# Performance work log

Measured on AMD Instinct MI355X. Metric: run time of the kernel, lower is better.

The kernel has to match this reference:

```python
import jax, jax.numpy as jnp
import numpy as np

N_NODES = 50000
N_EDGES = 800000
N_FEAT = 128
HIDDEN = 256
N_GRAPHS = 256
N_CLASSES = 10
BN_EPS = 1e-5


def setup_inputs() -> dict:
    key = jax.random.key(0)
    ks = jax.random.split(key, 12)
    s = 1.0 / np.sqrt(HIDDEN)
    inp = {
        "x": jax.random.normal(ks[0], (N_NODES, N_FEAT), dtype=jnp.float32),
        "edge_index": jax.random.randint(ks[1], (2, N_EDGES), 0, N_NODES, dtype=jnp.int64),
        "batch": jnp.sort(jax.random.randint(ks[2], (N_NODES,), 0, N_GRAPHS, dtype=jnp.int64)),
        "conv1_w0": jax.random.normal(ks[3], (N_FEAT, HIDDEN), dtype=jnp.float32) / np.sqrt(N_FEAT),
        "conv1_b0": jnp.zeros((HIDDEN,), jnp.float32),
        "conv1_w1": jax.random.normal(ks[4], (HIDDEN, HIDDEN), dtype=jnp.float32) * s,
        "conv1_b1": jnp.zeros((HIDDEN,), jnp.float32),
        "conv1_bn_gamma": jnp.ones((HIDDEN,), jnp.float32),
        "conv1_bn_beta": jnp.zeros((HIDDEN,), jnp.float32),
        "conv1_bn_mean": jnp.zeros((HIDDEN,), jnp.float32),
        "conv1_bn_var": jnp.ones((HIDDEN,), jnp.float32),
        "convs_w0": jax.random.normal(ks[5], (3, HIDDEN, HIDDEN), dtype=jnp.float32) * s,
        "convs_b0": jnp.zeros((3, HIDDEN), jnp.float32),
        "convs_w1": jax.random.normal(ks[6], (3, HIDDEN, HIDDEN), dtype=jnp.float32) * s,
        "convs_b1": jnp.zeros((3, HIDDEN), jnp.float32),
        "convs_bn_gamma": jnp.ones((3, HIDDEN), jnp.float32),
        "convs_bn_beta": jnp.zeros((3, HIDDEN), jnp.float32),
        "convs_bn_mean": jnp.zeros((3, HIDDEN), jnp.float32),
        "convs_bn_var": jnp.ones((3, HIDDEN), jnp.float32),
        "eps": jnp.zeros((4,), jnp.float32),
        "lin1_w": jax.random.normal(ks[7], (HIDDEN, HIDDEN), dtype=jnp.float32) * s,
        "lin1_b": jnp.zeros((HIDDEN,), jnp.float32),
        "lin2_w": jax.random.normal(ks[8], (HIDDEN, N_CLASSES), dtype=jnp.float32) * s,
        "lin2_b": jnp.zeros((N_CLASSES,), jnp.float32),
    }
    return inp


def _gin_conv(x, src, dst, eps, w0, b0, w1, b1, g, be, m, v):
    # message = x[src]; aggregate = scatter_add at dst; update = MLP((1+eps)*x + aggr)
    aggr = jax.ops.segment_sum(x[src], dst, num_segments=N_NODES)
    h = (1.0 + eps) * x + aggr
    h = jax.nn.relu(h @ w0 + b0)
    h = jax.nn.relu(h @ w1 + b1)
    return (h - m) * jax.lax.rsqrt(v + BN_EPS) * g + be  # eval-mode BatchNorm1d


def reference(x, edge_index, batch,
              conv1_w0, conv1_b0, conv1_w1, conv1_b1,
              conv1_bn_gamma, conv1_bn_beta, conv1_bn_mean, conv1_bn_var,
              convs_w0, convs_b0, convs_w1, convs_b1,
              convs_bn_gamma, convs_bn_beta, convs_bn_mean, convs_bn_var,
              eps, lin1_w, lin1_b, lin2_w, lin2_b):
    src, dst = edge_index[0], edge_index[1]
    h = _gin_conv(x, src, dst, eps[0], conv1_w0, conv1_b0, conv1_w1, conv1_b1,
                  conv1_bn_gamma, conv1_bn_beta, conv1_bn_mean, conv1_bn_var)
    for i in range(convs_w0.shape[0]):
        h = _gin_conv(h, src, dst, eps[i + 1], convs_w0[i], convs_b0[i],
                      convs_w1[i], convs_b1[i], convs_bn_gamma[i], convs_bn_beta[i],
                      convs_bn_mean[i], convs_bn_var[i])
    # global_mean_pool over graph ids
    sums = jax.ops.segment_sum(h, batch, num_segments=N_GRAPHS)
    cnts = jax.ops.segment_sum(jnp.ones((N_NODES,), h.dtype), batch, num_segments=N_GRAPHS)
    pooled = sums / jnp.maximum(cnts, 1.0)[:, None]
    h = jax.nn.relu(pooled @ lin1_w + lin1_b)  # dropout is identity at inference
    logits = h @ lin2_w + lin2_b
    return jax.nn.log_softmax(logits, axis=-1)
```

## Files before the change

### kernel.cpp

```cpp
#include <hip/hip_runtime.h>
#include <hip/hip_bf16.h>

#define N_NODES 50000
#define N_EDGES 800000
#define N_FEAT 128
#define HIDDEN 256
#define N_GRAPHS 256
#define N_CLASSES 10

#define NBUCK ((N_NODES + 255) / 256)
#define EPB 2048
#define NBLK_S ((N_EDGES + EPB - 1) / EPB)

typedef __hip_bfloat16 bf16_t;
typedef short bf16x8 __attribute__((ext_vector_type(8)));
typedef float f32x4 __attribute__((ext_vector_type(4)));

__device__ inline float bfb2f(short s) {
    unsigned u = ((unsigned)(unsigned short)s) << 16;
    float f; __builtin_memcpy(&f, &u, 4); return f;
}
__device__ inline short f2bfb(float f) {
    bf16_t b = __float2bfloat16(f);
    short s; __builtin_memcpy(&s, &b, 2); return s;
}


__global__ __launch_bounds__(256) void bucket_hist_kernel(const int* __restrict__ ei,
                                                          unsigned* __restrict__ histG) {
    __shared__ unsigned lh[NBUCK];
    int t = threadIdx.x, j = blockIdx.x;
    for (int i = t; i < NBUCK; i += 256) lh[i] = 0;
    __syncthreads();
    int base = j * EPB;
    #pragma unroll
    for (int it = 0; it < EPB / 256; it++) {
        int e = base + it * 256 + t;
        if (e < N_EDGES) atomicAdd(&lh[(unsigned)ei[N_EDGES + e] >> 8], 1u);
    }
    __syncthreads();
    for (int i = t; i < NBUCK; i += 256) histG[(size_t)j * NBUCK + i] = lh[i];
}

__global__ __launch_bounds__(256) void bucket_scan_kernel(unsigned* __restrict__ histG,
                                                          unsigned* __restrict__ bucketBase) {
    __shared__ unsigned tmp[256];
    int t = threadIdx.x;
    unsigned run = 0;
    if (t < NBUCK) {
        for (int j = 0; j < NBLK_S; j++) {
            unsigned v = histG[(size_t)j * NBUCK + t];
            histG[(size_t)j * NBUCK + t] = run;
            run += v;
        }
    }
    unsigned v = (t < NBUCK) ? run : 0;
    tmp[t] = v;
    __syncthreads();
    for (int off = 1; off < 256; off <<= 1) {
        unsigned a = (t >= off) ? tmp[t - off] : 0u;
        __syncthreads();
        tmp[t] += a;
        __syncthreads();
    }
    unsigned base = tmp[t] - v;
    if (t < NBUCK) {
        bucketBase[t] = base;
        for (int j = 0; j < NBLK_S; j++) histG[(size_t)j * NBUCK + t] += base;
    }
    if (t == NBUCK - 1) bucketBase[NBUCK] = base + v;
}

__global__ __launch_bounds__(256) void bucket_scatter_kernel(const int* __restrict__ ei,
                                                             const unsigned* __restrict__ histG,
                                                             unsigned long long* __restrict__ ebuf) {
    __shared__ unsigned lcur[NBUCK];
    int t = threadIdx.x, j = blockIdx.x;
    for (int i = t; i < NBUCK; i += 256) lcur[i] = histG[(size_t)j * NBUCK + i];
    __syncthreads();
    int base = j * EPB;
    #pragma unroll
    for (int it = 0; it < EPB / 256; it++) {
        int e = base + it * 256 + t;
        if (e < N_EDGES) {
            unsigned src = (unsigned)ei[e];
            unsigned dst = (unsigned)ei[N_EDGES + e];
            unsigned pos = atomicAdd(&lcur[dst >> 8], 1u);
            ebuf[pos] = (unsigned long long)src | ((unsigned long long)dst << 32);
        }
    }
}

__global__ __launch_bounds__(256) void fine_fill_kernel(const unsigned long long* __restrict__ ebuf,
                                                        const unsigned* __restrict__ bucketBase,
                                                        unsigned* __restrict__ rowptr,
                                                        int* __restrict__ adj) {
    __shared__ unsigned ldeg[256], lcur[256], tmp[256];
    int b = blockIdx.x, t = threadIdx.x;
    unsigned sbase = bucketBase[b];
    int scnt = (int)(bucketBase[b + 1] - sbase);
    ldeg[t] = 0;
    __syncthreads();
    for (int k = t; k < scnt; k += 256) {
        unsigned dst = (unsigned)(ebuf[sbase + k] >> 32);
        atomicAdd(&ldeg[dst & 255], 1u);
    }
    __syncthreads();
    unsigned v = ldeg[t];
    tmp[t] = v;
    __syncthreads();
    for (int off = 1; off < 256; off <<= 1) {
        unsigned a = (t >= off) ? tmp[t - off] : 0u;
        __syncthreads();
        tmp[t] += a;
        __syncthreads();
    }
    unsigned exc = tmp[t] - v;
    lcur[t] = exc;
    int gnode = b * 256 + t;
    if (gnode < N_NODES) rowptr[gnode] = sbase + exc;
    if (b == NBUCK - 1 && t == 0) rowptr[N_NODES] = N_EDGES;
    __syncthreads();
    for (int k = t; k < scnt; k += 256) {
        unsigned long long p = ebuf[sbase + k];
        unsigned dst = (unsigned)(p >> 32);
        unsigned pos = atomicAdd(&lcur[dst & 255], 1u);
        adj[sbase + pos] = (int)(p & 0xffffffffu);
    }
}


__global__ __launch_bounds__(256) void convert_x_kernel(const float* __restrict__ x,
                                                        bf16_t* __restrict__ xb) {
    int i = blockIdx.x * 256 + threadIdx.x;
    if (i < N_NODES * N_FEAT / 4) {
        float4 v = reinterpret_cast<const float4*>(x)[i];
        short4 o;
        o.x = f2bfb(v.x); o.y = f2bfb(v.y); o.z = f2bfb(v.z); o.w = f2bfb(v.w);
        reinterpret_cast<short4*>(xb)[i] = o;
    }
}


__global__ __launch_bounds__(256) void prep_weights_kernel(
    const float* __restrict__ c1_w0, const float* __restrict__ c1_w1,
    const float* __restrict__ cs_w0, const float* __restrict__ cs_w1,
    bf16_t* __restrict__ wt)
{
    __shared__ float T[32][33];
    int z = blockIdx.z;
    const float* src; int K; size_t off;
    if (z == 0)      { src = c1_w0; K = N_FEAT;  off = 0; }
    else if (z == 1) { src = c1_w1; K = HIDDEN;  off = 32768; }
    else {
        int i = (z - 2) >> 1;
        src = (((z - 2) & 1) ? cs_w1 : cs_w0) + (size_t)i * HIDDEN * HIDDEN;
        K = HIDDEN;
        off = 32768 + (size_t)(z - 1) * 65536;
    }
    int k0 = blockIdx.x * 32, n0 = blockIdx.y * 32;
    if (k0 >= K) return;
    int t = threadIdx.x;
    int r = t >> 3, c4 = (t & 7) * 4;
    float4 v = *reinterpret_cast<const float4*>(src + (size_t)(k0 + r) * HIDDEN + n0 + c4);
    T[r][c4 + 0] = v.x; T[r][c4 + 1] = v.y; T[r][c4 + 2] = v.z; T[r][c4 + 3] = v.w;
    __syncthreads();
    int n = t >> 3, kc = (t & 7) * 4;
    short4 o;
    o.x = f2bfb(T[kc + 0][n]); o.y = f2bfb(T[kc + 1][n]);
    o.z = f2bfb(T[kc + 2][n]); o.w = f2bfb(T[kc + 3][n]);
    *reinterpret_cast<short4*>((short*)wt + off + (size_t)(n0 + n) * K + k0 + kc) = o;
}


__global__ __launch_bounds__(256) void aggregate1_kernel(
    const bf16_t* __restrict__ xb, const int* __restrict__ adj,
    const unsigned* __restrict__ rowptr, const float* __restrict__ eps_arr,
    bf16_t* __restrict__ out)
{
    int w = threadIdx.x >> 6, lane = threadIdx.x & 63;
    int n = blockIdx.x * 4 + w;
    if (n >= N_NODES) return;
    int q = lane >> 4, l4 = lane & 15;
    unsigned beg = rowptr[n], end = rowptr[n + 1];
    const short* xs = (const short*)xb;
    float acc[8] = {};
    unsigned e = beg;
    for (; e + 8 <= end; e += 8) {
        int s0 = adj[e + q];
        int s1 = adj[e + 4 + q];
        bf16x8 v0 = *reinterpret_cast<const bf16x8*>(xs + (unsigned)s0 * N_FEAT + l4 * 8);
        bf16x8 v1 = *reinterpret_cast<const bf16x8*>(xs + (unsigned)s1 * N_FEAT + l4 * 8);
        #pragma unroll
        for (int j = 0; j < 8; j++) acc[j] += bfb2f(v0[j]) + bfb2f(v1[j]);
    }
    for (; e + 4 <= end; e += 4) {
        int s0 = adj[e + q];
        bf16x8 v0 = *reinterpret_cast<const bf16x8*>(xs + (unsigned)s0 * N_FEAT + l4 * 8);
        #pragma unroll
        for (int j = 0; j < 8; j++) acc[j] += bfb2f(v0[j]);
    }
    int rem = (int)(end - e);
    if (q < rem) {
        bf16x8 v0 = *reinterpret_cast<const bf16x8*>(xs + (unsigned)adj[e + q] * N_FEAT + l4 * 8);
        #pragma unroll
        for (int j = 0; j < 8; j++) acc[j] += bfb2f(v0[j]);
    }
    if (q == 0) {
        bf16x8 sv = *reinterpret_cast<const bf16x8*>(xs + (unsigned)n * N_FEAT + l4 * 8);
        float ep = 1.f + eps_arr[0];
        #pragma unroll
        for (int j = 0; j < 8; j++) acc[j] += ep * bfb2f(sv[j]);
    }
    #pragma unroll
    for (int j = 0; j < 8; j++) {
        acc[j] += __shfl_xor(acc[j], 16);
        acc[j] += __shfl_xor(acc[j], 32);
    }
    if (lane < 16) {
        bf16x8 o;
        #pragma unroll
        for (int j = 0; j < 8; j++) o[j] = f2bfb(acc[j]);
        *reinterpret_cast<bf16x8*>((short*)out + (unsigned)n * N_FEAT + l4 * 8) = o;
    }
}


__global__ __launch_bounds__(256) void aggregate2_kernel(
    const bf16_t* __restrict__ x, const int* __restrict__ adj,
    const unsigned* __restrict__ rowptr, const float* __restrict__ eps_arr, int eps_idx,
    bf16_t* __restrict__ out)
{
    int w = threadIdx.x >> 6, lane = threadIdx.x & 63;
    int n = blockIdx.x * 4 + w;
    if (n >= N_NODES) return;
    int half = lane >> 5, l5 = lane & 31;
    unsigned beg = rowptr[n], end = rowptr[n + 1];
    const short* xs = (const short*)x;
    float acc[8] = {};
    unsigned e = beg;
    for (; e + 8 <= end; e += 8) {
        int s0 = adj[e + half];
        int s1 = adj[e + 2 + half];
        int s2 = adj[e + 4 + half];
        int s3 = adj[e + 6 + half];
        bf16x8 v0 = *reinterpret_cast<const bf16x8*>(xs + (unsigned)s0 * HIDDEN + l5 * 8);
        bf16x8 v1 = *reinterpret_cast<const bf16x8*>(xs + (unsigned)s1 * HIDDEN + l5 * 8);
        bf16x8 v2 = *reinterpret_cast<const bf16x8*>(xs + (unsigned)s2 * HIDDEN + l5 * 8);
        bf16x8 v3 = *reinterpret_cast<const bf16x8*>(xs + (unsigned)s3 * HIDDEN + l5 * 8);
        #pragma unroll
        for (int j = 0; j < 8; j++)
            acc[j] += (bfb2f(v0[j]) + bfb2f(v1[j])) + (bfb2f(v2[j]) + bfb2f(v3[j]));
    }
    for (; e + 2 <= end; e += 2) {
        int s0 = adj[e + half];
        bf16x8 v0 = *reinterpret_cast<const bf16x8*>(xs + (unsigned)s0 * HIDDEN + l5 * 8);
        #pragma unroll
        for (int j = 0; j < 8; j++) acc[j] += bfb2f(v0[j]);
    }
    if (e < end && half == 0) {
        bf16x8 v0 = *reinterpret_cast<const bf16x8*>(xs + (unsigned)adj[e] * HIDDEN + l5 * 8);
        #pragma unroll
        for (int j = 0; j < 8; j++) acc[j] += bfb2f(v0[j]);
    }
    if (half == 0) {
        bf16x8 sv = *reinterpret_cast<const bf16x8*>(xs + (unsigned)n * HIDDEN + l5 * 8);
        float ep = 1.f + eps_arr[eps_idx];
        #pragma unroll
        for (int j = 0; j < 8; j++) acc[j] += ep * bfb2f(sv[j]);
    }
    #pragma unroll
    for (int j = 0; j < 8; j++) acc[j] += __shfl_xor(acc[j], 32);
    if (half == 0) {
        bf16x8 o;
        #pragma unroll
        for (int j = 0; j < 8; j++) o[j] = f2bfb(acc[j]);
        *reinterpret_cast<bf16x8*>((short*)out + (unsigned)n * HIDDEN + l5 * 8) = o;
    }
}


#define GBM 128
#define GBN 128
#define GBK 64

__global__ __launch_bounds__(512) void gemm_bf16_kernel(
    const bf16_t* __restrict__ A, const bf16_t* __restrict__ Wt,
    const float* __restrict__ bias, bf16_t* __restrict__ C,
    int M, int K,
    const float* __restrict__ bn_g, const float* __restrict__ bn_b,
    const float* __restrict__ bn_m, const float* __restrict__ bn_v, int do_bn)
{
    __shared__ short lds[18432];
    short (*As)[72] = reinterpret_cast<short(*)[72]>(lds);
    short (*Bs)[72] = reinterpret_cast<short(*)[72]>(lds + 9216);
    short (*Cs)[136] = reinterpret_cast<short(*)[136]>(lds);

    int tid = threadIdx.x;
    int lane = tid & 63;
    int wave = tid >> 6;
    int wr = wave >> 2, wc = wave & 3;
    int row0 = blockIdx.x * GBM, col0 = blockIdx.y * GBN;

    int lrow = tid >> 3, lch = tid & 7;

    const short* Ab = (const short*)A;
    const short* Wb = (const short*)Wt;

    f32x4 acc[4][2] = {};

    for (int k0 = 0; k0 < K; k0 += GBK) {
        #pragma unroll
        for (int rr = 0; rr < 2; rr++) {
            int r = lrow + rr * 64;
            int arow = row0 + r;
            bf16x8 av = {};
            if (arow < M)
                av = *reinterpret_cast<const bf16x8*>(Ab + (size_t)arow * K + k0 + lch * 8);
            *reinterpret_cast<bf16x8*>(&As[r][lch * 8]) = av;
            bf16x8 bv = *reinterpret_cast<const bf16x8*>(Wb + (size_t)(col0 + r) * K + k0 + lch * 8);
            *reinterpret_cast<bf16x8*>(&Bs[r][lch * 8]) = bv;
        }
        __syncthreads();

        int fr = lane & 15, fk = (lane >> 4) * 8;
        #pragma unroll
        for (int ks = 0; ks < 2; ks++) {
            bf16x8 a[4], b[2];
            #pragma unroll
            for (int m = 0; m < 4; m++)
                a[m] = *reinterpret_cast<const bf16x8*>(&As[wr * 64 + m * 16 + fr][ks * 32 + fk]);
            #pragma unroll
            for (int n = 0; n < 2; n++)
                b[n] = *reinterpret_cast<const bf16x8*>(&Bs[wc * 32 + n * 16 + fr][ks * 32 + fk]);
            #pragma unroll
            for (int m = 0; m < 4; m++)
                #pragma unroll
                for (int n = 0; n < 2; n++)
                    acc[m][n] = __builtin_amdgcn_mfma_f32_16x16x32_bf16(a[m], b[n], acc[m][n], 0, 0, 0);
        }
        __syncthreads();
    }

    #pragma unroll
    for (int m = 0; m < 4; m++) {
        #pragma unroll
        for (int n = 0; n < 2; n++) {
            int rl = wr * 64 + m * 16 + (lane >> 4) * 4;
            int cl = wc * 32 + n * 16 + (lane & 15);
            int c = col0 + cl;
            float bi = bias[c];
            #pragma unroll
            for (int r = 0; r < 4; r++) {
                float v = acc[m][n][r] + bi;
                v = fmaxf(v, 0.f);
                if (do_bn) v = (v - bn_m[c]) * rsqrtf(bn_v[c] + 1e-5f) * bn_g[c] + bn_b[c];
                Cs[rl + r][cl] = f2bfb(v);
            }
        }
    }
    __syncthreads();
    int lr = tid >> 2, c16 = tid & 3;
    int r = row0 + lr;
    if (r < M) {
        short* Cb = (short*)C;
        #pragma unroll
        for (int cc = 0; cc < 4; cc++) {
            int ch = c16 + cc * 4;
            bf16x8 cv = *reinterpret_cast<const bf16x8*>(&Cs[lr][ch * 8]);
            *reinterpret_cast<bf16x8*>(Cb + (size_t)r * HIDDEN + col0 + ch * 8) = cv;
        }
    }
}


__global__ __launch_bounds__(256) void pool_kernel(const bf16_t* __restrict__ h,
                                                   const int* __restrict__ batch,
                                                   float* __restrict__ pooled) {
    __shared__ int sbs[2];
    __shared__ float red[4][HIDDEN];
    int g = blockIdx.x;
    if (threadIdx.x == 0) {
        int lo = 0, hi = N_NODES;
        while (lo < hi) { int mid = (lo + hi) >> 1; if (batch[mid] < g) lo = mid + 1; else hi = mid; }
        sbs[0] = lo;
        hi = N_NODES;
        while (lo < hi) { int mid = (lo + hi) >> 1; if (batch[mid] < g + 1) lo = mid + 1; else hi = mid; }
        sbs[1] = lo;
    }
    __syncthreads();
    int sbeg = sbs[0], send = sbs[1];
    int w = threadIdx.x >> 6, lane = threadIdx.x & 63;
    int half = lane >> 5, l5 = lane & 31;
    const short* hb = (const short*)h;
    float acc[8] = {};
    for (int n = sbeg + w * 2 + half; n < send; n += 8) {
        bf16x8 v = *reinterpret_cast<const bf16x8*>(hb + (size_t)n * HIDDEN + l5 * 8);
        #pragma unroll
        for (int j = 0; j < 8; j++) acc[j] += bfb2f(v[j]);
    }
    #pragma unroll
    for (int j = 0; j < 8; j++) acc[j] += __shfl_xor(acc[j], 32);
    if (half == 0) {
        #pragma unroll
        for (int j = 0; j < 8; j++) red[w][l5 * 8 + j] = acc[j];
    }
    __syncthreads();
    int t = threadIdx.x;
    float s = red[0][t] + red[1][t] + red[2][t] + red[3][t];
    float cnt = (float)(send - sbeg);
    pooled[g * HIDDEN + t] = s / fmaxf(cnt, 1.f);
}


__global__ void head_kernel(const float* __restrict__ pooled,
                            const float* __restrict__ w1, const float* __restrict__ b1,
                            const float* __restrict__ w2, const float* __restrict__ b2,
                            float* __restrict__ out) {
    int g = blockIdx.x, t = threadIdx.x;
    __shared__ float p[HIDDEN];
    __shared__ float h1[HIDDEN];
    __shared__ float lg[N_CLASSES];
    p[t] = pooled[g * HIDDEN + t];
    __syncthreads();
    float acc = b1[t];
    for (int k = 0; k < HIDDEN; k++) acc += p[k] * w1[k * HIDDEN + t];
    h1[t] = fmaxf(acc, 0.f);
    __syncthreads();
    if (t < N_CLASSES) {
        float a = b2[t];
        for (int k = 0; k < HIDDEN; k++) a += h1[k] * w2[k * N_CLASSES + t];
        lg[t] = a;
    }
    __syncthreads();
    if (t == 0) {
        float mx = lg[0];
        for (int j = 1; j < N_CLASSES; j++) mx = fmaxf(mx, lg[j]);
        float se = 0.f;
        for (int j = 0; j < N_CLASSES; j++) se += expf(lg[j] - mx);
        float lse = mx + logf(se);
        for (int j = 0; j < N_CLASSES; j++) out[g * N_CLASSES + j] = lg[j] - lse;
    }
}


extern "C" void kernel_launch(void* const* d_in, const int* in_sizes, int n_in,
                              void* d_out, int out_size, void* d_ws, size_t ws_size,
                              hipStream_t stream) {
    const float* x       = (const float*)d_in[0];
    const int*   ei      = (const int*)d_in[1];
    const int*   batch   = (const int*)d_in[2];
    const float* c1_w0   = (const float*)d_in[3];
    const float* c1_b0   = (const float*)d_in[4];
    const float* c1_w1   = (const float*)d_in[5];
    const float* c1_b1   = (const float*)d_in[6];
    const float* c1_g    = (const float*)d_in[7];
    const float* c1_be   = (const float*)d_in[8];
    const float* c1_m    = (const float*)d_in[9];
    const float* c1_v    = (const float*)d_in[10];
    const float* cs_w0   = (const float*)d_in[11];
    const float* cs_b0   = (const float*)d_in[12];
    const float* cs_w1   = (const float*)d_in[13];
    const float* cs_b1   = (const float*)d_in[14];
    const float* cs_g    = (const float*)d_in[15];
    const float* cs_be   = (const float*)d_in[16];
    const float* cs_m    = (const float*)d_in[17];
    const float* cs_v    = (const float*)d_in[18];
    const float* eps     = (const float*)d_in[19];
    const float* lin1_w  = (const float*)d_in[20];
    const float* lin1_b  = (const float*)d_in[21];
    const float* lin2_w  = (const float*)d_in[22];
    const float* lin2_b  = (const float*)d_in[23];

    char* ws = (char*)d_ws;
    size_t off = 0;
    auto alloc = [&](size_t bytes) -> void* {
        void* p = ws + off;
        off += (bytes + 255) & ~(size_t)255;
        return p;
    };

    unsigned* histG      = (unsigned*)alloc((size_t)NBLK_S * NBUCK * 4);
    unsigned* bucketBase = (unsigned*)alloc((NBUCK + 1) * 4);
    unsigned long long* ebuf = (unsigned long long*)alloc((size_t)N_EDGES * 8);
    unsigned* rowptr     = (unsigned*)alloc((N_NODES + 1) * 4);
    int*      adj        = (int*)alloc(N_EDGES * 4);
    bf16_t*   Wt         = (bf16_t*)alloc((size_t)(32768 + 7 * 65536) * 2);
    bf16_t*   xb         = (bf16_t*)alloc((size_t)N_NODES * N_FEAT * 2);
    bf16_t*   B1         = (bf16_t*)alloc((size_t)N_NODES * HIDDEN * 2);
    bf16_t*   B2         = (bf16_t*)alloc((size_t)N_NODES * HIDDEN * 2);
    bf16_t*   B3         = (bf16_t*)alloc((size_t)N_NODES * HIDDEN * 2);
    float*    pooled     = (float*)alloc(N_GRAPHS * HIDDEN * 4);

    bf16_t* wt_10 = Wt;
    bf16_t* wt_11 = Wt + 32768;
    auto wt_c0 = [&](int i) { return Wt + 32768 + (size_t)(1 + 2 * i) * 65536; };
    auto wt_c1 = [&](int i) { return Wt + 32768 + (size_t)(2 + 2 * i) * 65536; };

    bucket_hist_kernel<<<NBLK_S, 256, 0, stream>>>(ei, histG);
    bucket_scan_kernel<<<1, 256, 0, stream>>>(histG, bucketBase);
    bucket_scatter_kernel<<<NBLK_S, 256, 0, stream>>>(ei, histG, ebuf);
    fine_fill_kernel<<<NBUCK, 256, 0, stream>>>(ebuf, bucketBase, rowptr, adj);

    convert_x_kernel<<<(N_NODES * N_FEAT / 4 + 255) / 256, 256, 0, stream>>>(x, xb);
    prep_weights_kernel<<<dim3(8, 8, 8), 256, 0, stream>>>(c1_w0, c1_w1, cs_w0, cs_w1, Wt);

    dim3 ggrid((N_NODES + GBM - 1) / GBM, HIDDEN / GBN);
    int ab = (N_NODES + 3) / 4;

    aggregate1_kernel<<<ab, 256, 0, stream>>>(xb, adj, rowptr, eps, B1);
    gemm_bf16_kernel<<<ggrid, 512, 0, stream>>>(B1, wt_10, c1_b0, B2, N_NODES, N_FEAT,
                                                nullptr, nullptr, nullptr, nullptr, 0);
    gemm_bf16_kernel<<<ggrid, 512, 0, stream>>>(B2, wt_11, c1_b1, B3, N_NODES, HIDDEN,
                                                c1_g, c1_be, c1_m, c1_v, 1);

    for (int i = 0; i < 3; i++) {
        aggregate2_kernel<<<ab, 256, 0, stream>>>(B3, adj, rowptr, eps, i + 1, B1);
        gemm_bf16_kernel<<<ggrid, 512, 0, stream>>>(B1, wt_c0(i), cs_b0 + i * HIDDEN, B2,
                                                    N_NODES, HIDDEN,
                                                    nullptr, nullptr, nullptr, nullptr, 0);
        gemm_bf16_kernel<<<ggrid, 512, 0, stream>>>(B2, wt_c1(i), cs_b1 + i * HIDDEN, B3,
                                                    N_NODES, HIDDEN,
                                                    cs_g + i * HIDDEN, cs_be + i * HIDDEN,
                                                    cs_m + i * HIDDEN, cs_v + i * HIDDEN, 1);
    }

    pool_kernel<<<N_GRAPHS, 256, 0, stream>>>(B3, batch, pooled);
    head_kernel<<<N_GRAPHS, HIDDEN, 0, stream>>>(pooled, lin1_w, lin1_b, lin2_w, lin2_b, (float*)d_out);
}
```

Measured before the change: 514.6 us.

## Parallelize bucket prefix scan across buckets with transposed histogram layout

Replaces the single-block serial scan over 391 edge blocks per bucket with a per-bucket block-parallel scan over a transposed histogram, followed by a small scan over bucket totals. The scatter kernel then adds the bucket base when loading its cursors. This removes a long serial, single-workgroup loop from the CSR build path, at the cost of one extra kernel launch and strided writes in the histogram kernel.

```diff
diff --git a/kernel.cpp b/kernel.cpp
--- a/kernel.cpp
+++ b/kernel.cpp
@@ -27,7 +27,7 @@
 
 
 __global__ __launch_bounds__(256) void bucket_hist_kernel(const int* __restrict__ ei,
-                                                          unsigned* __restrict__ histG) {
+                                                          unsigned* __restrict__ histT) {
     __shared__ unsigned lh[NBUCK];
     int t = threadIdx.x, j = blockIdx.x;
     for (int i = t; i < NBUCK; i += 256) lh[i] = 0;
@@ -39,44 +39,59 @@
         if (e < N_EDGES) atomicAdd(&lh[(unsigned)ei[N_EDGES + e] >> 8], 1u);
     }
     __syncthreads();
-    for (int i = t; i < NBUCK; i += 256) histG[(size_t)j * NBUCK + i] = lh[i];
-}
-
-__global__ __launch_bounds__(256) void bucket_scan_kernel(unsigned* __restrict__ histG,
-                                                          unsigned* __restrict__ bucketBase) {
+    for (int i = t; i < NBUCK; i += 256) histT[(size_t)i * NBLK_S + j] = lh[i];
+}
+
+__global__ __launch_bounds__(256) void bucket_scan_a_kernel(unsigned* __restrict__ histT,
+                                                            unsigned* __restrict__ bucketTot) {
+    __shared__ unsigned tmp[256];
+    int b = blockIdx.x, t = threadIdx.x;
+    unsigned* row = histT + (size_t)b * NBLK_S;
+    int i0 = t * 2, i1 = t * 2 + 1;
+    unsigned v0 = (i0 < NBLK_S) ? row[i0] : 0u;
+    unsigned v1 = (i1 < NBLK_S) ? row[i1] : 0u;
+    unsigned s = v0 + v1;
+    tmp[t] = s;
+    __syncthreads();
+    #pragma unroll
+    for (int off = 1; off < 256; off <<= 1) {
+        unsigned a = (t >= off) ? tmp[t - off] : 0u;
+        __syncthreads();
+        tmp[t] += a;
+        __syncthreads();
+    }
+    unsigned base = tmp[t] - s;
+    if (i0 < NBLK_S) row[i0] = base;
+    if (i1 < NBLK_S) row[i1] = base + v0;
+    if (t == 255) bucketTot[b] = tmp[255];
+}
+
+__global__ __launch_bounds__(256) void bucket_scan_b_kernel(const unsigned* __restrict__ bucketTot,
+                                                            unsigned* __restrict__ bucketBase) {
     __shared__ unsigned tmp[256];
     int t = threadIdx.x;
-    unsigned run = 0;
-    if (t < NBUCK) {
-        for (int j = 0; j < NBLK_S; j++) {
-            unsigned v = histG[(size_t)j * NBUCK + t];
-            histG[(size_t)j * NBUCK + t] = run;
-            run += v;
-        }
-    }
-    unsigned v = (t < NBUCK) ? run : 0;
+    unsigned v = (t < NBUCK) ? bucketTot[t] : 0u;
     tmp[t] = v;
     __syncthreads();
+    #pragma unroll
     for (int off = 1; off < 256; off <<= 1) {
         unsigned a = (t >= off) ? tmp[t - off] : 0u;
         __syncthreads();
         tmp[t] += a;
         __syncthreads();
     }
-    unsigned base = tmp[t] - v;
-    if (t < NBUCK) {
-        bucketBase[t] = base;
-        for (int j = 0; j < NBLK_S; j++) histG[(size_t)j * NBUCK + t] += base;
-    }
-    if (t == NBUCK - 1) bucketBase[NBUCK] = base + v;
+    if (t < NBUCK) bucketBase[t] = tmp[t] - v;
+    if (t == NBUCK - 1) bucketBase[NBUCK] = tmp[t];
 }
 
 __global__ __launch_bounds__(256) void bucket_scatter_kernel(const int* __restrict__ ei,
-                                                             const unsigned* __restrict__ histG,
+                                                             const unsigned* __restrict__ histT,
+                                                             const unsigned* __restrict__ bucketBase,
                                                              unsigned long long* __restrict__ ebuf) {
     __shared__ unsigned lcur[NBUCK];
     int t = threadIdx.x, j = blockIdx.x;
-    for (int i = t; i < NBUCK; i += 256) lcur[i] = histG[(size_t)j * NBUCK + i];
+    for (int i = t; i < NBUCK; i += 256)
+        lcur[i] = histT[(size_t)i * NBLK_S + j] + bucketBase[i];
     __syncthreads();
     int base = j * EPB;
     #pragma unroll
@@ -480,7 +495,8 @@
         return p;
     };
 
-    unsigned* histG      = (unsigned*)alloc((size_t)NBLK_S * NBUCK * 4);
+    unsigned* histT      = (unsigned*)alloc((size_t)NBUCK * NBLK_S * 4);
+    unsigned* bucketTot  = (unsigned*)alloc(NBUCK * 4);
     unsigned* bucketBase = (unsigned*)alloc((NBUCK + 1) * 4);
     unsigned long long* ebuf = (unsigned long long*)alloc((size_t)N_EDGES * 8);
     unsigned* rowptr     = (unsigned*)alloc((N_NODES + 1) * 4);
@@ -497,9 +513,10 @@
     auto wt_c0 = [&](int i) { return Wt + 32768 + (size_t)(1 + 2 * i) * 65536; };
     auto wt_c1 = [&](int i) { return Wt + 32768 + (size_t)(2 + 2 * i) * 65536; };
 
-    bucket_hist_kernel<<<NBLK_S, 256, 0, stream>>>(ei, histG);
-    bucket_scan_kernel<<<1, 256, 0, stream>>>(histG, bucketBase);
-    bucket_scatter_kernel<<<NBLK_S, 256, 0, stream>>>(ei, histG, ebuf);
+    bucket_hist_kernel<<<NBLK_S, 256, 0, stream>>>(ei, histT);
+    bucket_scan_a_kernel<<<NBUCK, 256, 0, stream>>>(histT, bucketTot);
+    bucket_scan_b_kernel<<<1, 256, 0, stream>>>(bucketTot, bucketBase);
+    bucket_scatter_kernel<<<NBLK_S, 256, 0, stream>>>(ei, histT, bucketBase, ebuf);
     fine_fill_kernel<<<NBUCK, 256, 0, stream>>>(ebuf, bucketBase, rowptr, adj);
 
     convert_x_kernel<<<(N_NODES * N_FEAT / 4 + 255) / 256, 256, 0, stream>>>(x, xb);
```

New measurement: 460.9 us. 1.12x faster.
